# Kernel optimization log

Measured on AMD Instinct MI355X. Metric: run time of the kernel, lower is better.

The kernel has to match this reference:

```python
import jax, jax.numpy as jnp
import numpy as np

# cfg constants (ProposalLayerSoft.__init__)
GRID_SIZE = jnp.array([8000.0, 8000.0, 2000.0], dtype=jnp.float32)   # MULTI_PERSON.SPACE_SIZE (mm)
CUBE_SIZE = jnp.array([128.0, 128.0, 64.0], dtype=jnp.float32)       # MULTI_PERSON.INITIAL_CUBE_SIZE
GRID_CENTER = jnp.array([0.0, 0.0, 300.0], dtype=jnp.float32)        # MULTI_PERSON.SPACE_CENTER
NUM_CAND = 10                                                         # MULTI_PERSON.MAX_PEOPLE_NUM
THRESHOLD = 0.3                                                       # MULTI_PERSON.THRESHOLD


def setup_inputs() -> dict:
    key = jax.random.key(0)
    # root heatmap cube in [0,1): [B, X, Y, Z]
    root_cubes = jax.random.uniform(key, (32, 128, 128, 64), dtype=jnp.float32)
    return {"root_cubes": root_cubes}


def _nms_topk(x):
    """3x3x3 max-pool peak suppression + top-k (repo's nms()).
    x: [B, X, Y, Z] -> (values [B,K], unravel_index [B,K,3] float)."""
    B, X, Y, Z = x.shape
    pooled = jax.lax.reduce_window(
        x, -jnp.inf, jax.lax.max,
        window_dimensions=(1, 3, 3, 3),
        window_strides=(1, 1, 1, 1),
        padding=[(0, 0), (1, 1), (1, 1), (1, 1)],
    )
    peaks = jnp.where(x == pooled, x, 0.0)           # keep only local maxima
    flat = peaks.reshape(B, X * Y * Z)
    topk_values, topk_index = jax.lax.top_k(flat, NUM_CAND)
    # C-order unravel (matches repo's get_index)
    ix = topk_index // (Y * Z)
    iy = (topk_index % (Y * Z)) // Z
    iz = topk_index % Z
    idx = jnp.stack([ix, iy, iz], axis=-1).astype(jnp.float32)  # [B, K, 3]
    return topk_values, idx


def reference(root_cubes):
    x = jax.lax.stop_gradient(root_cubes)  # original calls .detach()
    topk_values, topk_index = _nms_topk(x)
    # get_real_loc: voxel index -> world coords (mm)
    loc = topk_index / (CUBE_SIZE - 1.0) * GRID_SIZE + GRID_CENTER - GRID_SIZE / 2.0
    conf = (topk_values > THRESHOLD).astype(jnp.float32) - 1.0  # col 3
    grid_centers = jnp.concatenate(
        [loc, conf[..., None], topk_values[..., None]], axis=-1
    )  # [B, K, 5]: (x, y, z, valid_flag, score)
    return grid_centers
```

## Files before the change

### kernel.cpp

```cpp
#include <hip/hip_runtime.h>
#include <stdint.h>


#define TPB 256
#define NK 10
#define TX 10
#define BLOCKS_PER_B (4 * TX)
#define WCAP 512
typedef unsigned long long u64;

__device__ __forceinline__ u64 bfly_max_u64(u64 v) {
#pragma unroll
  for (int off = 1; off < 64; off <<= 1) {
    u64 o = __shfl_xor(v, off, 64);
    v = (o > v) ? o : v;
  }
  return v;
}

__device__ __forceinline__ float dpp_nbr_a(float v) {
  return __int_as_float(__builtin_amdgcn_update_dpp(
      0, __float_as_int(v), 0x101, 0xF, 0xF, true));
}
__device__ __forceinline__ float dpp_nbr_b(float v) {
  return __int_as_float(__builtin_amdgcn_update_dpp(
      0, __float_as_int(v), 0x111, 0xF, 0xF, true));
}

__global__ __launch_bounds__(TPB, 5) void peaks_topk(
    const float* __restrict__ in, u64* __restrict__ part) {
  __shared__ u64 cand[4][WCAP];
  __shared__ u64 wtop[4 * NK];
  const int tid = threadIdx.x;
  const int w = tid >> 6, lane = tid & 63;
  const int xi = lane & 15, zq = lane >> 4;
  const int tx = blockIdx.x, b = blockIdx.z;
  const int seg = blockIdx.y * 4 + w;
  const int x0 = tx * 14 - 1;
  const int gx = x0 + xi;
  const int cx = min(127, max(0, gx));
  const int y0 = seg * 8;
  const bool emit_ok = (xi >= 1) && (xi <= 14) && (gx <= 127);
  const float* __restrict__ col =
      in + ((size_t)b << 20) + ((size_t)cx << 13) + (zq << 4);

  int wcnt = 0;
  float vb[3][16], zmb[3][16];

  auto loadv = [&](int y, float* v) {
    const int cy = min(127, max(0, y));
    const float4* p = (const float4*)(col + ((size_t)cy << 6));
    float4 a = p[0], bb = p[1], c = p[2], d = p[3];
    v[0] = a.x;  v[1] = a.y;  v[2] = a.z;  v[3] = a.w;
    v[4] = bb.x; v[5] = bb.y; v[6] = bb.z; v[7] = bb.w;
    v[8] = c.x;  v[9] = c.y;  v[10] = c.z; v[11] = c.w;
    v[12] = d.x; v[13] = d.y; v[14] = d.z; v[15] = d.w;
  };
  auto zmcalc = [&](const float* v, float* zm) {
    float vl = __shfl_up(v[15], 16, 64);
    float vr = __shfl_down(v[0], 16, 64);
    vl = (zq == 0) ? -1e30f : vl;
    vr = (zq == 3) ? -1e30f : vr;
    zm[0] = fmaxf(vl, fmaxf(v[0], v[1]));
#pragma unroll
    for (int j = 1; j < 15; ++j)
      zm[j] = fmaxf(v[j - 1], fmaxf(v[j], v[j + 1]));
    zm[15] = fmaxf(v[14], fmaxf(v[15], vr));
  };

  loadv(y0 - 1, vb[2]);
  loadv(y0, vb[0]);
  loadv(y0 + 1, vb[1]);
  zmcalc(vb[2], zmb[2]);
  zmcalc(vb[0], zmb[0]);

#pragma unroll
  for (int t = 0; t < 8; ++t) {
    const int y = y0 + t;
    if (t < 7) loadv(y + 2, vb[(t + 2) % 3]);
    zmcalc(vb[(t + 1) % 3], zmb[(t + 1) % 3]);
    const float* vC = vb[t % 3];
    const float* zmP = zmb[(t + 2) % 3];
    const float* zmC = zmb[t % 3];
    const float* zmN = zmb[(t + 1) % 3];
#pragma unroll
    for (int j = 0; j < 16; ++j) {
      float ym = fmaxf(zmP[j], fmaxf(zmC[j], zmN[j]));
      float l = dpp_nbr_a(ym);
      float r = dpp_nbr_b(ym);
      float m27 = fmaxf(ym, fmaxf(l, r));
      float v = vC[j];
      const bool pred = emit_ok && (v >= m27);
      u64 mask = __ballot(pred);
      if (pred) {
        unsigned g = ((unsigned)gx << 13) | ((unsigned)y << 6) |
                     (unsigned)((zq << 4) + j);
        u64 key = ((u64)__float_as_uint(v) << 32) | (u64)(unsigned)(~g);
        int ofs = __builtin_amdgcn_mbcnt_hi(
            (unsigned)(mask >> 32),
            __builtin_amdgcn_mbcnt_lo((unsigned)mask, 0));
        int slot = wcnt + ofs;
        if (slot < WCAP) cand[w][slot] = key;
      }
      wcnt += (int)__popcll(mask);
    }
  }

  __builtin_amdgcn_s_waitcnt(0);
  const int count = min(wcnt, WCAP);
  u64 c[WCAP / 64];
#pragma unroll
  for (int i = 0; i < WCAP / 64; ++i) {
    int idx = lane + (i << 6);
    c[i] = (idx < count) ? cand[w][idx] : 0;
  }
  u64 mine = 0;
#pragma unroll 1
  for (int r = 0; r < NK; ++r) {
    u64 best = c[0];
#pragma unroll
    for (int i = 1; i < WCAP / 64; ++i) best = (c[i] > best) ? c[i] : best;
    u64 m = bfly_max_u64(best);
    if (m != 0 && best == m) {
#pragma unroll
      for (int i = 0; i < WCAP / 64; ++i)
        if (c[i] == m) c[i] = 0;
    }
    if (lane == r) mine = m;
  }
  if (lane < NK) wtop[w * NK + lane] = mine;
  __syncthreads();

  if (w == 0) {
    u64 c0 = (lane < 4 * NK) ? wtop[lane] : 0;
    u64 mv = 0;
#pragma unroll 1
    for (int r = 0; r < NK; ++r) {
      u64 m = bfly_max_u64(c0);
      if (m != 0 && c0 == m) c0 = 0;
      if (lane == r) mv = m;
    }
    if (lane < NK) {
      const int bi = blockIdx.y * TX + tx;
      part[((size_t)b * BLOCKS_PER_B + bi) * NK + lane] = mv;
    }
  }
}

__global__ __launch_bounds__(64) void final_select(
    const u64* __restrict__ part, float* __restrict__ out) {
  const int lane = threadIdx.x & 63;
  const int b = blockIdx.x;
  const int NKEY = BLOCKS_PER_B * NK;

  const u64* __restrict__ src = part + (size_t)b * NKEY;
  u64 c[7];
#pragma unroll
  for (int i = 0; i < 7; ++i) {
    int idx = lane + (i << 6);
    c[i] = (idx < NKEY) ? src[idx] : 0;
  }
  u64 mine = 0;
#pragma unroll 1
  for (int r = 0; r < NK; ++r) {
    u64 best = c[0];
#pragma unroll
    for (int i = 1; i < 7; ++i) best = (c[i] > best) ? c[i] : best;
    u64 m = bfly_max_u64(best);
    if (m != 0 && best == m) {
#pragma unroll
      for (int i = 0; i < 7; ++i)
        if (c[i] == m) c[i] = 0;
    }
    if (lane == r) mine = m;
  }
  if (lane < NK) {
    float val = 0.0f;
    unsigned g = 0u;
    if (mine != 0) {
      val = __uint_as_float((unsigned)(mine >> 32));
      g = ~((unsigned)mine);
    }
    float fx = (float)(g >> 13) * (8000.0f / 127.0f) - 4000.0f;
    float fy = (float)((g >> 6) & 127u) * (8000.0f / 127.0f) - 4000.0f;
    float fz = (float)(g & 63u) * (2000.0f / 63.0f) - 700.0f;
    float conf = (val > 0.3f) ? 0.0f : -1.0f;
    float* o = out + ((size_t)b * NK + lane) * 5;
    o[0] = fx; o[1] = fy; o[2] = fz; o[3] = conf; o[4] = val;
  }
}

extern "C" void kernel_launch(void* const* d_in, const int* in_sizes, int n_in,
                              void* d_out, int out_size, void* d_ws, size_t ws_size,
                              hipStream_t stream) {
  const float* in = (const float*)d_in[0];
  float* out = (float*)d_out;
  u64* part = (u64*)d_ws;

  const int B = in_sizes[0] >> 20;
  dim3 gridA(TX, 4, (unsigned)B);
  peaks_topk<<<gridA, dim3(TPB), 0, stream>>>(in, part);
  final_select<<<dim3((unsigned)B), dim3(64), 0, stream>>>(part, out);
}
```

Before: 219.2 us.

## Swap tile axes so lanes span y and stream along x for contiguous loads

Remaps the stencil tile so the 16 lanes of each wavefront cover consecutive y rows while each wavefront streams along x. A wavefront load now reads one contiguous 4 KB slab per x-slice instead of 16 scattered 256 B rows 32 KB apart, which should improve memory coalescing and DRAM page locality. The halo overlap moves from the x axis to the y axis. Launch bounds occupancy hint is lowered from 5 to 4, which may change register allocation.

```diff
diff --git a/kernel.cpp b/kernel.cpp
--- a/kernel.cpp
+++ b/kernel.cpp
@@ -4,8 +4,8 @@
 
 #define TPB 256
 #define NK 10
-#define TX 10
-#define BLOCKS_PER_B (4 * TX)
+#define TY 10
+#define BLOCKS_PER_B (4 * TY)
 #define WCAP 512
 typedef unsigned long long u64;
 
@@ -27,29 +27,29 @@
       0, __float_as_int(v), 0x111, 0xF, 0xF, true));
 }
 
-__global__ __launch_bounds__(TPB, 5) void peaks_topk(
+__global__ __launch_bounds__(TPB, 4) void peaks_topk(
     const float* __restrict__ in, u64* __restrict__ part) {
   __shared__ u64 cand[4][WCAP];
   __shared__ u64 wtop[4 * NK];
   const int tid = threadIdx.x;
   const int w = tid >> 6, lane = tid & 63;
-  const int xi = lane & 15, zq = lane >> 4;
-  const int tx = blockIdx.x, b = blockIdx.z;
+  const int yi = lane & 15, zq = lane >> 4;
+  const int ty = blockIdx.x, b = blockIdx.z;
   const int seg = blockIdx.y * 4 + w;
-  const int x0 = tx * 14 - 1;
-  const int gx = x0 + xi;
-  const int cx = min(127, max(0, gx));
-  const int y0 = seg * 8;
-  const bool emit_ok = (xi >= 1) && (xi <= 14) && (gx <= 127);
+  const int y0 = ty * 14 - 1;
+  const int gy = y0 + yi;
+  const int cy = min(127, max(0, gy));
+  const int x0 = seg * 8;
+  const bool emit_ok = (yi >= 1) && (yi <= 14) && (gy <= 127);
   const float* __restrict__ col =
-      in + ((size_t)b << 20) + ((size_t)cx << 13) + (zq << 4);
+      in + ((size_t)b << 20) + ((size_t)cy << 6) + (zq << 4);
 
   int wcnt = 0;
   float vb[3][16], zmb[3][16];
 
-  auto loadv = [&](int y, float* v) {
-    const int cy = min(127, max(0, y));
-    const float4* p = (const float4*)(col + ((size_t)cy << 6));
+  auto loadv = [&](int x, float* v) {
+    const int cx = min(127, max(0, x));
+    const float4* p = (const float4*)(col + ((size_t)cx << 13));
     float4 a = p[0], bb = p[1], c = p[2], d = p[3];
     v[0] = a.x;  v[1] = a.y;  v[2] = a.z;  v[3] = a.w;
     v[4] = bb.x; v[5] = bb.y; v[6] = bb.z; v[7] = bb.w;
@@ -68,16 +68,16 @@
     zm[15] = fmaxf(v[14], fmaxf(v[15], vr));
   };
 
-  loadv(y0 - 1, vb[2]);
-  loadv(y0, vb[0]);
-  loadv(y0 + 1, vb[1]);
+  loadv(x0 - 1, vb[2]);
+  loadv(x0, vb[0]);
+  loadv(x0 + 1, vb[1]);
   zmcalc(vb[2], zmb[2]);
   zmcalc(vb[0], zmb[0]);
 
 #pragma unroll
   for (int t = 0; t < 8; ++t) {
-    const int y = y0 + t;
-    if (t < 7) loadv(y + 2, vb[(t + 2) % 3]);
+    const int x = x0 + t;
+    if (t < 7) loadv(x + 2, vb[(t + 2) % 3]);
     zmcalc(vb[(t + 1) % 3], zmb[(t + 1) % 3]);
     const float* vC = vb[t % 3];
     const float* zmP = zmb[(t + 2) % 3];
@@ -85,15 +85,15 @@
     const float* zmN = zmb[(t + 1) % 3];
 #pragma unroll
     for (int j = 0; j < 16; ++j) {
-      float ym = fmaxf(zmP[j], fmaxf(zmC[j], zmN[j]));
-      float l = dpp_nbr_a(ym);
-      float r = dpp_nbr_b(ym);
-      float m27 = fmaxf(ym, fmaxf(l, r));
+      float xm = fmaxf(zmP[j], fmaxf(zmC[j], zmN[j]));
+      float l = dpp_nbr_a(xm);
+      float r = dpp_nbr_b(xm);
+      float m27 = fmaxf(xm, fmaxf(l, r));
       float v = vC[j];
       const bool pred = emit_ok && (v >= m27);
       u64 mask = __ballot(pred);
       if (pred) {
-        unsigned g = ((unsigned)gx << 13) | ((unsigned)y << 6) |
+        unsigned g = ((unsigned)x << 13) | ((unsigned)gy << 6) |
                      (unsigned)((zq << 4) + j);
         u64 key = ((u64)__float_as_uint(v) << 32) | (u64)(unsigned)(~g);
         int ofs = __builtin_amdgcn_mbcnt_hi(
@@ -141,7 +141,7 @@
       if (lane == r) mv = m;
     }
     if (lane < NK) {
-      const int bi = blockIdx.y * TX + tx;
+      const int bi = blockIdx.y * TY + ty;
       part[((size_t)b * BLOCKS_PER_B + bi) * NK + lane] = mv;
     }
   }
@@ -198,7 +198,7 @@
   u64* part = (u64*)d_ws;
 
   const int B = in_sizes[0] >> 20;
-  dim3 gridA(TX, 4, (unsigned)B);
+  dim3 gridA(TY, 4, (unsigned)B);
   peaks_topk<<<gridA, dim3(TPB), 0, stream>>>(in, part);
   final_select<<<dim3((unsigned)B), dim3(64), 0, stream>>>(part, out);
 }
```

New measurement: 213.5 us. 2.6% less time.
